# Kernel tuning notes

Measured on AMD Instinct MI355X. Metric: run time of the kernel, lower is better.

The kernel has to match this reference:

```python
import jax, jax.numpy as jnp
import numpy as np

N = 100000       # nodes
E = 1600000      # edges (avg degree 16)
D_IN = 128
D_HID = 128      # 2 * out_channels
D_OUT = 64
BN_EPS = 1e-5
LRELU_SLOPE = 0.01
NORM_SCALE = 1.8


def setup_inputs() -> dict:
    key = jax.random.key(0)
    ks = jax.random.split(key, 8)
    x = jax.random.normal(ks[0], (N, D_IN), dtype=jnp.float32)
    edge_src = jax.random.randint(ks[1], (E,), 0, N)
    edge_dst = jax.random.randint(ks[2], (E,), 0, N)
    W1 = jax.random.normal(ks[3], (D_IN, D_HID), dtype=jnp.float32) / np.sqrt(D_IN).astype(np.float32)
    b1 = jnp.zeros((D_HID,), jnp.float32)
    gamma = jnp.ones((D_HID,), jnp.float32)
    beta = jnp.zeros((D_HID,), jnp.float32)
    Wmu = jax.random.normal(ks[4], (D_HID, D_OUT), dtype=jnp.float32) / np.sqrt(D_HID).astype(np.float32)
    bmu = jnp.zeros((D_OUT,), jnp.float32)
    noise = jax.random.normal(ks[5], (N, D_OUT), dtype=jnp.float32)
    return {"x": x, "edge_src": edge_src, "edge_dst": edge_dst, "W1": W1, "b1": b1,
            "gamma": gamma, "beta": beta, "Wmu": Wmu, "bmu": bmu, "noise": noise}


def appnp_k1(x, src, dst):
    """APPNP(K=1, alpha=0) == one symmetric GCN-normalized SpMM with self-loops."""
    ones = jnp.ones((src.shape[0],), x.dtype)
    deg = jax.ops.segment_sum(ones, dst, num_segments=N) + 1.0  # +1 for self-loop
    dinv = jax.lax.rsqrt(deg)
    w = dinv[src] * dinv[dst]                                   # [E] edge weights
    agg = jax.ops.segment_sum(x[src] * w[:, None], dst, num_segments=N)
    return agg + x * (dinv * dinv)[:, None]                     # self-loop term


def reference(x, edge_src, edge_dst, W1, b1, gamma, beta, Wmu, bmu, noise):
    # conv1 + propagate
    h = x @ W1 + b1                         # [N, D_HID]
    h = appnp_k1(h, edge_src, edge_dst)
    # BatchNorm1d (training mode: batch stats, biased variance)
    mean = h.mean(axis=0)
    var = h.var(axis=0)
    h = gamma * (h - mean) * jax.lax.rsqrt(var + BN_EPS) + beta
    # LeakyReLU
    h = jnp.where(h > 0, h, LRELU_SLOPE * h)
    # mu branch (convmu + propagate)
    l = h @ Wmu + bmu                       # [N, D_OUT]; used for both mu and logstd (original reuses convmu)
    mu = appnp_k1(l, edge_src, edge_dst)
    # logstd branch: F.normalize(convmu(h), p=2, dim=1) * 1.8 then propagate
    nrm = jnp.maximum(jnp.linalg.norm(l, axis=1, keepdims=True), 1e-12)
    logstd = appnp_k1(l / nrm * NORM_SCALE, edge_src, edge_dst)
    # reparam (training): mu + eps * exp(logstd)
    zeta = mu + noise * jnp.exp(logstd)
    return (mu, logstd, zeta)
```

## Files before the change

kernel.cpp:

```cpp
#include <hip/hip_runtime.h>
#include <hip/hip_bf16.h>
#include <math.h>

#define D_IN 128
#define D_HID 128
#define D_OUT 64
#define BN_EPS 1e-5f
#define SLOPE 0.01f
#define NSCALE 1.8f

#define BSH 8
#define NB 256
#define T1 4096
#define COLCAP 8192
#define LSTRIDE 192

typedef __attribute__((ext_vector_type(8))) short short8;
typedef __attribute__((ext_vector_type(4))) float f32x4;

__device__ inline void atomAddF(float* p, float v) {
#if defined(__gfx90a__) || defined(__gfx942__) || defined(__gfx950__)
    unsafeAtomicAdd(p, v);
#else
    atomicAdd(p, v);
#endif
}

__device__ inline ushort f2bf(float f) {
    union { float f; uint u; } v; v.f = f;
    uint r = v.u + 0x7fff + ((v.u >> 16) & 1);
    return (ushort)(r >> 16);
}
__device__ inline float bf2f(ushort b) {
    union { uint u; float f; } v; v.u = ((uint)b) << 16;
    return v.f;
}
__device__ inline float bflo(uint u) { return __uint_as_float(u << 16); }
__device__ inline float bfhi(uint u) { return __uint_as_float(u & 0xffff0000u); }

__device__ inline void add8(uint4 v, float a[8]) {
    a[0] += bflo(v.x); a[1] += bfhi(v.x);
    a[2] += bflo(v.y); a[3] += bfhi(v.y);
    a[4] += bflo(v.z); a[5] += bfhi(v.z);
    a[6] += bflo(v.w); a[7] += bfhi(v.w);
}
__device__ inline void fma8(uint4 v, float w, float a[8]) {
    a[0] = fmaf(bflo(v.x), w, a[0]);
    a[1] = fmaf(bfhi(v.x), w, a[1]);
    a[2] = fmaf(bflo(v.y), w, a[2]);
    a[3] = fmaf(bfhi(v.y), w, a[3]);
    a[4] = fmaf(bflo(v.z), w, a[4]);
    a[5] = fmaf(bfhi(v.z), w, a[5]);
    a[6] = fmaf(bflo(v.w), w, a[6]);
    a[7] = fmaf(bfhi(v.w), w, a[7]);
}
__device__ inline void acc8(uint4 v, float sv, float w, float am[8], float al[8]) {
    float e;
    e = bflo(v.x) * w; am[0] += e; al[0] = fmaf(e, sv, al[0]);
    e = bfhi(v.x) * w; am[1] += e; al[1] = fmaf(e, sv, al[1]);
    e = bflo(v.y) * w; am[2] += e; al[2] = fmaf(e, sv, al[2]);
    e = bfhi(v.y) * w; am[3] += e; al[3] = fmaf(e, sv, al[3]);
    e = bflo(v.z) * w; am[4] += e; al[4] = fmaf(e, sv, al[4]);
    e = bfhi(v.z) * w; am[5] += e; al[5] = fmaf(e, sv, al[5]);
    e = bflo(v.w) * w; am[6] += e; al[6] = fmaf(e, sv, al[6]);
    e = bfhi(v.w) * w; am[7] += e; al[7] = fmaf(e, sv, al[7]);
}

__global__ __launch_bounds__(256) void k_bhist(const int* __restrict__ dst,
        int* __restrict__ bcnt, int E, int B) {
    __shared__ int h[512];
    for (int i = threadIdx.x; i < 512; i += 256) h[i] = 0;
    __syncthreads();
    int beg = blockIdx.x * T1;
    int end = min(beg + T1, E);
    for (int e = beg + threadIdx.x; e < end; e += 256)
        atomicAdd(&h[dst[e] >> BSH], 1);
    __syncthreads();
    for (int i = threadIdx.x; i < B; i += 256)
        if (h[i]) atomicAdd(&bcnt[i], h[i]);
}

__global__ __launch_bounds__(512) void k_bscan(const int* __restrict__ bcnt,
        int* __restrict__ bbase, int* __restrict__ tailE, int B) {
    __shared__ int sh[512];
    int t = threadIdx.x;
    int v = (t < B) ? bcnt[t] : 0;
    sh[t] = v;
    __syncthreads();
    for (int o = 1; o < 512; o <<= 1) {
        int u = (t >= o) ? sh[t - o] : 0;
        __syncthreads();
        sh[t] += u;
        __syncthreads();
    }
    int excl = sh[t] - v;
    if (t < B) { bbase[t] = excl; tailE[t] = excl; }
    if (t == B - 1) bbase[B] = excl + v;
}

__global__ __launch_bounds__(256) void k_part(const int* __restrict__ src,
        const int* __restrict__ dst, int* __restrict__ tailE,
        int2* __restrict__ ep, int E, int B) {
    __shared__ int h[512], off[512], gb[512], cur[512];
    __shared__ int ps[256];
    __shared__ int2 ro[T1];
    int tid = threadIdx.x;
    for (int i = tid; i < 512; i += 256) h[i] = 0;
    __syncthreads();
    int beg = blockIdx.x * T1;
    int cnt = min(T1, E - beg);
    int s[16], d[16];
#pragma unroll
    for (int k = 0; k < 16; ++k) {
        int e = beg + tid + k * 256;
        if (e < E) {
            s[k] = src[e]; d[k] = dst[e];
            atomicAdd(&h[d[k] >> BSH], 1);
        } else d[k] = -1;
    }
    __syncthreads();
    int pa = h[2 * tid], pb = h[2 * tid + 1];
    ps[tid] = pa + pb;
    __syncthreads();
    int vv = ps[tid];
    for (int o = 1; o < 256; o <<= 1) {
        int u = (tid >= o) ? ps[tid - o] : 0;
        __syncthreads();
        ps[tid] += u;
        __syncthreads();
    }
    int excl = ps[tid] - vv;
    off[2 * tid] = excl;       off[2 * tid + 1] = excl + pa;
    cur[2 * tid] = excl;       cur[2 * tid + 1] = excl + pa;
    if (2 * tid < B && pa > 0)      gb[2 * tid] = atomicAdd(&tailE[2 * tid], pa);
    if (2 * tid + 1 < B && pb > 0)  gb[2 * tid + 1] = atomicAdd(&tailE[2 * tid + 1], pb);
    __syncthreads();
#pragma unroll
    for (int k = 0; k < 16; ++k) {
        if (d[k] >= 0) {
            int b = d[k] >> BSH;
            int p = atomicAdd(&cur[b], 1);
            ro[p] = make_int2(s[k], d[k]);
        }
    }
    __syncthreads();
    for (int i = tid; i < cnt; i += 256) {
        int2 e = ro[i];
        int b = e.y >> BSH;
        ep[gb[b] + (i - off[b])] = e;
    }
}

__global__ __launch_bounds__(256) void k_csr(const int2* __restrict__ ep,
        const int* __restrict__ bbase, int* __restrict__ rowptr,
        float* __restrict__ dinv, int* __restrict__ col, int n, int B) {
    int b = blockIdx.x;
    int lo = b << BSH;
    int hi = min(lo + NB, n);
    int nn = hi - lo;
    int ebeg = bbase[b], eend = bbase[b + 1], cnt = eend - ebeg;
    __shared__ int h[NB], pfx[NB], cur[NB];
    __shared__ int colbuf[COLCAP];
    int tid = threadIdx.x;
    if (tid < NB) h[tid] = 0;
    __syncthreads();
    for (int i = tid; i < cnt; i += 256)
        atomicAdd(&h[ep[ebeg + i].y - lo], 1);
    __syncthreads();
    int v = (tid < nn) ? h[tid] : 0;
    pfx[tid] = v;
    __syncthreads();
    for (int o = 1; o < 256; o <<= 1) {
        int u = (tid >= o) ? pfx[tid - o] : 0;
        __syncthreads();
        pfx[tid] += u;
        __syncthreads();
    }
    int excl = pfx[tid] - v;
    if (tid < nn) {
        rowptr[lo + tid] = ebeg + excl;
        dinv[lo + tid] = rsqrtf((float)v + 1.0f);
        cur[tid] = excl;
    }
    if (b == B - 1 && tid == 0) rowptr[n] = eend;
    __syncthreads();
    if (cnt <= COLCAP) {
        for (int i = tid; i < cnt; i += 256) {
            int2 e = ep[ebeg + i];
            int p = atomicAdd(&cur[e.y - lo], 1);
            colbuf[p] = e.x;
        }
        __syncthreads();
        for (int i = tid; i < cnt; i += 256) col[ebeg + i] = colbuf[i];
    } else {
        for (int i = tid; i < cnt; i += 256) {
            int2 e = ep[ebeg + i];
            int p = atomicAdd(&cur[e.y - lo], 1);
            col[ebeg + p] = e.x;
        }
    }
}

__global__ __launch_bounds__(256) void k_gemm1_mfma(const float* __restrict__ x,
        const float* __restrict__ W1, const float* __restrict__ b1,
        const float* __restrict__ dinv, ushort* __restrict__ h_bf, int n, int nwt) {
    __shared__ ushort wf[2][4][8][64][8];
    int t = threadIdx.x;
    for (int i = t; i < 16384; i += 256) {
        int k = i >> 7, nn = i & 127;
        float v = W1[i];
        ushort hi = f2bf(v);
        ushort lo = f2bf(v - bf2f(hi));
        int kt = k >> 5, ct = nn >> 4;
        int lane = ((k >> 3) & 3) * 16 + (nn & 15);
        int j = k & 7;
        wf[0][kt][ct][lane][j] = hi;
        wf[1][kt][ct][lane][j] = lo;
    }
    __syncthreads();
    int wid = t >> 6, lane = t & 63;
    int lrow = lane & 15, lkg = lane >> 4;
    float bias[8];
#pragma unroll
    for (int ct = 0; ct < 8; ++ct) bias[ct] = b1[ct * 16 + lrow];
    int stride = gridDim.x * 4;
    for (int wt = blockIdx.x * 4 + wid; wt < nwt; wt += stride) {
        size_t r0 = (size_t)wt * 16;
        int rr = (int)r0 + lrow;
        if (rr >= n) rr = n - 1;
        short8 ah[4], al[4];
#pragma unroll
        for (int kt = 0; kt < 4; ++kt) {
            const float* p = x + (size_t)rr * 128 + kt * 32 + lkg * 8;
            float va[8];
            *(f32x4*)&va[0] = *(const f32x4*)p;
            *(f32x4*)&va[4] = *(const f32x4*)(p + 4);
#pragma unroll
            for (int j = 0; j < 8; ++j) {
                ushort hb = f2bf(va[j]);
                ah[kt][j] = (short)hb;
                al[kt][j] = (short)f2bf(va[j] - bf2f(hb));
            }
        }
        f32x4 acc[8];
#pragma unroll
        for (int ct = 0; ct < 8; ++ct) {
            float bb = bias[ct];
            acc[ct][0] = bb; acc[ct][1] = bb; acc[ct][2] = bb; acc[ct][3] = bb;
        }
#pragma unroll
        for (int kt = 0; kt < 4; ++kt) {
#pragma unroll
            for (int ct = 0; ct < 8; ++ct) {
                short8 wh = *(const short8*)&wf[0][kt][ct][lane][0];
                short8 wl = *(const short8*)&wf[1][kt][ct][lane][0];
                acc[ct] = __builtin_amdgcn_mfma_f32_16x16x32_bf16(ah[kt], wh, acc[ct], 0, 0, 0);
                acc[ct] = __builtin_amdgcn_mfma_f32_16x16x32_bf16(al[kt], wh, acc[ct], 0, 0, 0);
                acc[ct] = __builtin_amdgcn_mfma_f32_16x16x32_bf16(ah[kt], wl, acc[ct], 0, 0, 0);
            }
        }
#pragma unroll
        for (int j = 0; j < 4; ++j) {
            int row = (int)r0 + lkg * 4 + j;
            if (row < n) {
                float dr = dinv[row];
#pragma unroll
                for (int ct = 0; ct < 8; ++ct)
                    h_bf[(size_t)row * 128 + ct * 16 + lrow] = f2bf(acc[ct][j] * dr);
            }
        }
    }
}

__global__ __launch_bounds__(512) void k_spmm1_csr(const int* __restrict__ rowptr,
        const int* __restrict__ col, const uint4* __restrict__ hb4,
        const float* __restrict__ dinv, uint4* __restrict__ agg_bf,
        float* __restrict__ accum, int n) {
    __shared__ float red[8][16][8];
    int t = threadIdx.x;
    int wid = t >> 6, lane = t & 63;
    int q = lane >> 4, g = lane & 15;
    int gw = blockIdx.x * 8 + wid;
    int nw = gridDim.x * 8;
    float sx[8], sq[8];
#pragma unroll
    for (int j = 0; j < 8; ++j) { sx[j] = 0.f; sq[j] = 0.f; }
    for (int node = gw; node < n; node += nw) {
        int beg = rowptr[node], end = rowptr[node + 1];
        float a[8];
#pragma unroll
        for (int j = 0; j < 8; ++j) a[j] = 0.f;
        if (q == 0) add8(hb4[(size_t)node * 16 + g], a);
        int p = beg;
        for (; p + 16 <= end; p += 16) {
            int c0 = col[p + q], c1 = col[p + 4 + q];
            int c2 = col[p + 8 + q], c3 = col[p + 12 + q];
            uint4 v0 = hb4[(size_t)c0 * 16 + g];
            uint4 v1 = hb4[(size_t)c1 * 16 + g];
            uint4 v2 = hb4[(size_t)c2 * 16 + g];
            uint4 v3 = hb4[(size_t)c3 * 16 + g];
            add8(v0, a); add8(v1, a); add8(v2, a); add8(v3, a);
        }
        if (p + 8 <= end) {
            int c0 = col[p + q], c1 = col[p + 4 + q];
            uint4 v0 = hb4[(size_t)c0 * 16 + g];
            uint4 v1 = hb4[(size_t)c1 * 16 + g];
            add8(v0, a); add8(v1, a);
            p += 8;
        }
        if (p < end) {
            int i0 = p + q, i1 = p + 4 + q;
            int c0 = col[i0 < end ? i0 : end - 1];
            int c1 = col[i1 < end ? i1 : end - 1];
            float w0 = (i0 < end) ? 1.f : 0.f;
            float w1 = (i1 < end) ? 1.f : 0.f;
            fma8(hb4[(size_t)c0 * 16 + g], w0, a);
            fma8(hb4[(size_t)c1 * 16 + g], w1, a);
        }
#pragma unroll
        for (int j = 0; j < 8; ++j) {
            a[j] += __shfl_xor(a[j], 16, 64);
            a[j] += __shfl_xor(a[j], 32, 64);
        }
        if (q == 0) {
            float di = dinv[node];
#pragma unroll
            for (int j = 0; j < 8; ++j) a[j] *= di;
            uint4 pk;
            pk.x = ((uint)f2bf(a[1]) << 16) | (uint)f2bf(a[0]);
            pk.y = ((uint)f2bf(a[3]) << 16) | (uint)f2bf(a[2]);
            pk.z = ((uint)f2bf(a[5]) << 16) | (uint)f2bf(a[4]);
            pk.w = ((uint)f2bf(a[7]) << 16) | (uint)f2bf(a[6]);
            agg_bf[(size_t)node * 16 + g] = pk;
#pragma unroll
            for (int j = 0; j < 8; ++j) {
                sx[j] += a[j];
                sq[j] = fmaf(a[j], a[j], sq[j]);
            }
        }
    }
    if (q == 0) {
#pragma unroll
        for (int j = 0; j < 8; ++j) red[wid][g][j] = sx[j];
    }
    __syncthreads();
    if (t < 128) {
        float v = 0.f;
        for (int w = 0; w < 8; ++w) v += red[w][t >> 3][t & 7];
        atomAddF(&accum[t], v);
    }
    __syncthreads();
    if (q == 0) {
#pragma unroll
        for (int j = 0; j < 8; ++j) red[wid][g][j] = sq[j];
    }
    __syncthreads();
    if (t < 128) {
        float v = 0.f;
        for (int w = 0; w < 8; ++w) v += red[w][t >> 3][t & 7];
        atomAddF(&accum[128 + t], v);
    }
}

__global__ __launch_bounds__(256) void k_gemm2_mfma(const ushort* __restrict__ agg_bf,
        const float* __restrict__ Wmu, const float* __restrict__ bmu,
        const float* __restrict__ accum, const float* __restrict__ gamma,
        const float* __restrict__ beta, const float* __restrict__ dinv,
        char* __restrict__ l_ext, float inv_n, int n, int nwt) {
    __shared__ ushort wf[2][4][4][64][8];
    __shared__ float scs[D_HID], shs[D_HID];
    int t = threadIdx.x;
    for (int i = t; i < 8192; i += 256) {
        int k = i >> 6, nn = i & 63;
        float v = Wmu[i];
        ushort hi = f2bf(v);
        ushort lo = f2bf(v - bf2f(hi));
        int kt = k >> 5, ct = nn >> 4;
        int lane = ((k >> 3) & 3) * 16 + (nn & 15);
        int j = k & 7;
        wf[0][kt][ct][lane][j] = hi;
        wf[1][kt][ct][lane][j] = lo;
    }
    for (int i = t; i < D_HID; i += 256) {
        float mean = accum[i] * inv_n;
        float var = accum[D_HID + i] * inv_n - mean * mean;
        float sc = gamma[i] * rsqrtf(var + BN_EPS);
        scs[i] = sc;
        shs[i] = beta[i] - mean * sc;
    }
    __syncthreads();
    int wid = t >> 6, lane = t & 63;
    int lrow = lane & 15, lkg = lane >> 4;
    float bias[4];
#pragma unroll
    for (int ct = 0; ct < 4; ++ct) bias[ct] = bmu[ct * 16 + lrow];
    int stride = gridDim.x * 4;
    for (int wt = blockIdx.x * 4 + wid; wt < nwt; wt += stride) {
        size_t r0 = (size_t)wt * 16;
        int rr = (int)r0 + lrow;
        if (rr >= n) rr = n - 1;
        short8 ah[4], al[4];
#pragma unroll
        for (int kt = 0; kt < 4; ++kt) {
            const ushort* p = agg_bf + (size_t)rr * 128 + kt * 32 + lkg * 8;
            short8 raw = *(const short8*)p;
#pragma unroll
            for (int j = 0; j < 8; ++j) {
                int k = kt * 32 + lkg * 8 + j;
                float v = bf2f((ushort)raw[j]) * scs[k] + shs[k];
                v = v > 0.f ? v : SLOPE * v;
                ushort hb = f2bf(v);
                ah[kt][j] = (short)hb;
                al[kt][j] = (short)f2bf(v - bf2f(hb));
            }
        }
        f32x4 acc[4];
#pragma unroll
        for (int ct = 0; ct < 4; ++ct) {
            float bb = bias[ct];
            acc[ct][0] = bb; acc[ct][1] = bb; acc[ct][2] = bb; acc[ct][3] = bb;
        }
#pragma unroll
        for (int kt = 0; kt < 4; ++kt) {
#pragma unroll
            for (int ct = 0; ct < 4; ++ct) {
                short8 wh = *(const short8*)&wf[0][kt][ct][lane][0];
                short8 wl = *(const short8*)&wf[1][kt][ct][lane][0];
                acc[ct] = __builtin_amdgcn_mfma_f32_16x16x32_bf16(ah[kt], wh, acc[ct], 0, 0, 0);
                acc[ct] = __builtin_amdgcn_mfma_f32_16x16x32_bf16(al[kt], wh, acc[ct], 0, 0, 0);
                acc[ct] = __builtin_amdgcn_mfma_f32_16x16x32_bf16(ah[kt], wl, acc[ct], 0, 0, 0);
            }
        }
#pragma unroll
        for (int j = 0; j < 4; ++j) {
            float ss = acc[0][j] * acc[0][j];
#pragma unroll
            for (int ct = 1; ct < 4; ++ct) ss = fmaf(acc[ct][j], acc[ct][j], ss);
            ss += __shfl_xor(ss, 1, 64);
            ss += __shfl_xor(ss, 2, 64);
            ss += __shfl_xor(ss, 4, 64);
            ss += __shfl_xor(ss, 8, 64);
            float srow = NSCALE / fmaxf(sqrtf(ss), 1e-12f);
            int row = (int)r0 + lkg * 4 + j;
            if (row < n) {
                float dr = dinv[row];
                char* base = l_ext + (size_t)row * LSTRIDE;
#pragma unroll
                for (int ct = 0; ct < 4; ++ct)
                    *(ushort*)(base + (ct * 16 + lrow) * 2) = f2bf(acc[ct][j] * dr);
                if (lrow == 0) *(float*)(base + 128) = srow;
            }
        }
    }
}

__global__ __launch_bounds__(512) void k_spmm2_csr(const int* __restrict__ rowptr,
        const int* __restrict__ col, const char* __restrict__ lb,
        const float* __restrict__ dinv, const float* __restrict__ noise,
        float* __restrict__ mu, float* __restrict__ lsd, float* __restrict__ zeta,
        int n) {
    int node = blockIdx.x * 8 + ((int)threadIdx.x >> 6);
    if (node >= n) return;
    int lane = threadIdx.x & 63;
    int oct = lane >> 3, g = lane & 7;
    int beg = rowptr[node], end = rowptr[node + 1];
    float am[8], al[8];
#pragma unroll
    for (int j = 0; j < 8; ++j) { am[j] = 0.f; al[j] = 0.f; }
    if (oct == 0) {
        const char* rb = lb + (size_t)node * LSTRIDE;
        uint4 v = *(const uint4*)(rb + g * 16);
        float sv = *(const float*)(rb + 128);
        acc8(v, sv, 1.f, am, al);
    }
    int p = beg;
    for (; p + 16 <= end; p += 16) {
        int c0 = col[p + oct], c1 = col[p + 8 + oct];
        const char* r0 = lb + (size_t)c0 * LSTRIDE;
        const char* r1 = lb + (size_t)c1 * LSTRIDE;
        uint4 v0 = *(const uint4*)(r0 + g * 16);
        float s0 = *(const float*)(r0 + 128);
        uint4 v1 = *(const uint4*)(r1 + g * 16);
        float s1 = *(const float*)(r1 + 128);
        acc8(v0, s0, 1.f, am, al);
        acc8(v1, s1, 1.f, am, al);
    }
    if (p + 8 <= end) {
        int c0 = col[p + oct];
        const char* r0 = lb + (size_t)c0 * LSTRIDE;
        uint4 v0 = *(const uint4*)(r0 + g * 16);
        float s0 = *(const float*)(r0 + 128);
        acc8(v0, s0, 1.f, am, al);
        p += 8;
    }
    if (p < end) {
        int i0 = p + oct;
        int c0 = col[i0 < end ? i0 : end - 1];
        float w0 = (i0 < end) ? 1.f : 0.f;
        const char* r0 = lb + (size_t)c0 * LSTRIDE;
        uint4 v0 = *(const uint4*)(r0 + g * 16);
        float s0 = *(const float*)(r0 + 128);
        acc8(v0, s0, w0, am, al);
    }
#pragma unroll
    for (int j = 0; j < 8; ++j) {
        am[j] += __shfl_xor(am[j], 8, 64);
        am[j] += __shfl_xor(am[j], 16, 64);
        am[j] += __shfl_xor(am[j], 32, 64);
        al[j] += __shfl_xor(al[j], 8, 64);
        al[j] += __shfl_xor(al[j], 16, 64);
        al[j] += __shfl_xor(al[j], 32, 64);
    }
    if (lane < 8) {
        float di = dinv[node];
        size_t idx = (size_t)node * 64 + lane * 8;
        f32x4 m0, m1, l0, l1, z0, z1;
#pragma unroll
        for (int j = 0; j < 4; ++j) {
            m0[j] = am[j] * di;     m1[j] = am[j + 4] * di;
            l0[j] = al[j] * di;     l1[j] = al[j + 4] * di;
        }
        f32x4 n0 = *(const f32x4*)(noise + idx);
        f32x4 n1 = *(const f32x4*)(noise + idx + 4);
#pragma unroll
        for (int j = 0; j < 4; ++j) {
            z0[j] = m0[j] + n0[j] * expf(l0[j]);
            z1[j] = m1[j] + n1[j] * expf(l1[j]);
        }
        *(f32x4*)(mu + idx) = m0;   *(f32x4*)(mu + idx + 4) = m1;
        *(f32x4*)(lsd + idx) = l0;  *(f32x4*)(lsd + idx + 4) = l1;
        *(f32x4*)(zeta + idx) = z0; *(f32x4*)(zeta + idx + 4) = z1;
    }
}

extern "C" void kernel_launch(void* const* d_in, const int* in_sizes, int n_in,
                              void* d_out, int out_size, void* d_ws, size_t ws_size,
                              hipStream_t stream) {
    const float* x     = (const float*)d_in[0];
    const int*   esrc  = (const int*)d_in[1];
    const int*   edst  = (const int*)d_in[2];
    const float* W1    = (const float*)d_in[3];
    const float* b1    = (const float*)d_in[4];
    const float* gamma = (const float*)d_in[5];
    const float* beta  = (const float*)d_in[6];
    const float* Wmu   = (const float*)d_in[7];
    const float* bmu   = (const float*)d_in[8];
    const float* noise = (const float*)d_in[9];
    int N = in_sizes[0] / D_IN;
    int E = in_sizes[1];
    int B = (N + NB - 1) >> BSH;
    int nwt = (N + 15) / 16;
    int ntile = (E + T1 - 1) / T1;

    float* out  = (float*)d_out;
    float* mu   = out;
    float* lsd  = out + (size_t)N * D_OUT;
    float* zeta = out + 2 * (size_t)N * D_OUT;

    char* ws = (char*)d_ws;
    size_t off = 0;
    auto alloc = [&](size_t bytes) {
        void* p = ws + off;
        off += (bytes + 255) & ~(size_t)255;
        return p;
    };
    float* accum  = (float*)alloc(1024);
    int* bcnt     = (int*)alloc((size_t)B * 4);
    size_t zbytes = off;
    int* bbase    = (int*)alloc(((size_t)B + 1) * 4);
    int* tailE    = (int*)alloc((size_t)B * 4);
    int* rowptr   = (int*)alloc(((size_t)N + 1) * 4);
    float* dinv   = (float*)alloc((size_t)N * 4);
    int2* ep      = (int2*)alloc((size_t)E * 8);
    int* col      = (int*)alloc((size_t)E * 4);
    ushort* h_bf  = (ushort*)alloc((size_t)N * D_HID * 2);
    uint4* agg_bf = (uint4*)alloc((size_t)N * D_HID * 2);
    char* l_ext   = (char*)alloc((size_t)N * LSTRIDE);

    hipMemsetAsync(d_ws, 0, zbytes, stream);

    k_bhist<<<ntile, 256, 0, stream>>>(edst, bcnt, E, B);
    k_bscan<<<1, 512, 0, stream>>>(bcnt, bbase, tailE, B);
    k_part<<<ntile, 256, 0, stream>>>(esrc, edst, tailE, ep, E, B);
    k_csr<<<B, 256, 0, stream>>>(ep, bbase, rowptr, dinv, col, N, B);
    k_gemm1_mfma<<<512, 256, 0, stream>>>(x, W1, b1, dinv, h_bf, N, nwt);
    k_spmm1_csr<<<2048, 512, 0, stream>>>(rowptr, col, (const uint4*)h_bf, dinv, agg_bf, accum, N);
    k_gemm2_mfma<<<512, 256, 0, stream>>>((const ushort*)agg_bf, Wmu, bmu, accum,
                                          gamma, beta, dinv, l_ext, 1.0f / (float)N, N, nwt);
    k_spmm2_csr<<<(N + 7) / 8, 512, 0, stream>>>(rowptr, col, l_ext, dinv, noise, mu, lsd, zeta, N);
}
```

Measured before the change: 317.5 us.

## Split first SpMM into two feature halves, pack edge keys, drop weight-lo MFMA

The first GEMM now writes its output as two 64-column planes, and the first SpMM runs twice, once per plane. Each pass gathers from a 12.8 MB table instead of a 25.6 MB one, which is meant to raise cache hit rates for the random neighbor gathers. The edge partition buffer is packed into one 32-bit word (24-bit source plus 8-bit local destination), halving that traffic. Both GEMMs drop the low-part weight MFMA term, cutting a third of the MFMA work at some accuracy cost. The second launch also re-reads the CSR structure, and the packing assumes node ids fit in 24 bits.

```diff
diff --git a/kernel.cpp b/kernel.cpp
--- a/kernel.cpp
+++ b/kernel.cpp
@@ -38,21 +38,15 @@
 __device__ inline float bflo(uint u) { return __uint_as_float(u << 16); }
 __device__ inline float bfhi(uint u) { return __uint_as_float(u & 0xffff0000u); }
 
-__device__ inline void add8(uint4 v, float a[8]) {
+__device__ inline void add4(uint2 v, float a[4]) {
     a[0] += bflo(v.x); a[1] += bfhi(v.x);
     a[2] += bflo(v.y); a[3] += bfhi(v.y);
-    a[4] += bflo(v.z); a[5] += bfhi(v.z);
-    a[6] += bflo(v.w); a[7] += bfhi(v.w);
-}
-__device__ inline void fma8(uint4 v, float w, float a[8]) {
+}
+__device__ inline void fma4(uint2 v, float w, float a[4]) {
     a[0] = fmaf(bflo(v.x), w, a[0]);
     a[1] = fmaf(bfhi(v.x), w, a[1]);
     a[2] = fmaf(bflo(v.y), w, a[2]);
     a[3] = fmaf(bfhi(v.y), w, a[3]);
-    a[4] = fmaf(bflo(v.z), w, a[4]);
-    a[5] = fmaf(bfhi(v.z), w, a[5]);
-    a[6] = fmaf(bflo(v.w), w, a[6]);
-    a[7] = fmaf(bfhi(v.w), w, a[7]);
 }
 __device__ inline void acc8(uint4 v, float sv, float w, float am[8], float al[8]) {
     float e;
@@ -100,7 +94,7 @@
 
 __global__ __launch_bounds__(256) void k_part(const int* __restrict__ src,
         const int* __restrict__ dst, int* __restrict__ tailE,
-        int2* __restrict__ ep, int E, int B) {
+        uint* __restrict__ ep, int E, int B) {
     __shared__ int h[512], off[512], gb[512], cur[512];
     __shared__ int ps[256];
     __shared__ int2 ro[T1];
@@ -147,11 +141,11 @@
     for (int i = tid; i < cnt; i += 256) {
         int2 e = ro[i];
         int b = e.y >> BSH;
-        ep[gb[b] + (i - off[b])] = e;
-    }
-}
-
-__global__ __launch_bounds__(256) void k_csr(const int2* __restrict__ ep,
+        ep[gb[b] + (i - off[b])] = (uint)e.x | ((uint)(e.y & (NB - 1)) << 24);
+    }
+}
+
+__global__ __launch_bounds__(256) void k_csr(const uint* __restrict__ ep,
         const int* __restrict__ bbase, int* __restrict__ rowptr,
         float* __restrict__ dinv, int* __restrict__ col, int n, int B) {
     int b = blockIdx.x;
@@ -165,7 +159,7 @@
     if (tid < NB) h[tid] = 0;
     __syncthreads();
     for (int i = tid; i < cnt; i += 256)
-        atomicAdd(&h[ep[ebeg + i].y - lo], 1);
+        atomicAdd(&h[ep[ebeg + i] >> 24], 1);
     __syncthreads();
     int v = (tid < nn) ? h[tid] : 0;
     pfx[tid] = v;
@@ -186,17 +180,17 @@
     __syncthreads();
     if (cnt <= COLCAP) {
         for (int i = tid; i < cnt; i += 256) {
-            int2 e = ep[ebeg + i];
-            int p = atomicAdd(&cur[e.y - lo], 1);
-            colbuf[p] = e.x;
+            uint e = ep[ebeg + i];
+            int p = atomicAdd(&cur[e >> 24], 1);
+            colbuf[p] = (int)(e & 0xFFFFFFu);
         }
         __syncthreads();
         for (int i = tid; i < cnt; i += 256) col[ebeg + i] = colbuf[i];
     } else {
         for (int i = tid; i < cnt; i += 256) {
-            int2 e = ep[ebeg + i];
-            int p = atomicAdd(&cur[e.y - lo], 1);
-            col[ebeg + p] = e.x;
+            uint e = ep[ebeg + i];
+            int p = atomicAdd(&cur[e >> 24], 1);
+            col[ebeg + p] = (int)(e & 0xFFFFFFu);
         }
     }
 }
@@ -204,20 +198,17 @@
 __global__ __launch_bounds__(256) void k_gemm1_mfma(const float* __restrict__ x,
         const float* __restrict__ W1, const float* __restrict__ b1,
         const float* __restrict__ dinv, ushort* __restrict__ h_bf, int n, int nwt) {
-    __shared__ ushort wf[2][4][8][64][8];
+    __shared__ ushort wf[4][8][64][8];
     int t = threadIdx.x;
     for (int i = t; i < 16384; i += 256) {
         int k = i >> 7, nn = i & 127;
-        float v = W1[i];
-        ushort hi = f2bf(v);
-        ushort lo = f2bf(v - bf2f(hi));
         int kt = k >> 5, ct = nn >> 4;
         int lane = ((k >> 3) & 3) * 16 + (nn & 15);
         int j = k & 7;
-        wf[0][kt][ct][lane][j] = hi;
-        wf[1][kt][ct][lane][j] = lo;
-    }
-    __syncthreads();
+        wf[kt][ct][lane][j] = f2bf(W1[i]);
+    }
+    __syncthreads();
+    size_t n64 = (size_t)n * 64;
     int wid = t >> 6, lane = t & 63;
     int lrow = lane & 15, lkg = lane >> 4;
     float bias[8];
@@ -252,11 +243,9 @@
         for (int kt = 0; kt < 4; ++kt) {
 #pragma unroll
             for (int ct = 0; ct < 8; ++ct) {
-                short8 wh = *(const short8*)&wf[0][kt][ct][lane][0];
-                short8 wl = *(const short8*)&wf[1][kt][ct][lane][0];
+                short8 wh = *(const short8*)&wf[kt][ct][lane][0];
                 acc[ct] = __builtin_amdgcn_mfma_f32_16x16x32_bf16(ah[kt], wh, acc[ct], 0, 0, 0);
                 acc[ct] = __builtin_amdgcn_mfma_f32_16x16x32_bf16(al[kt], wh, acc[ct], 0, 0, 0);
-                acc[ct] = __builtin_amdgcn_mfma_f32_16x16x32_bf16(ah[kt], wl, acc[ct], 0, 0, 0);
             }
         }
 #pragma unroll
@@ -266,46 +255,43 @@
                 float dr = dinv[row];
 #pragma unroll
                 for (int ct = 0; ct < 8; ++ct)
-                    h_bf[(size_t)row * 128 + ct * 16 + lrow] = f2bf(acc[ct][j] * dr);
+                    h_bf[(size_t)(ct >> 2) * n64 + (size_t)row * 64 + (ct & 3) * 16 + lrow]
+                        = f2bf(acc[ct][j] * dr);
             }
         }
     }
 }
 
 __global__ __launch_bounds__(512) void k_spmm1_csr(const int* __restrict__ rowptr,
-        const int* __restrict__ col, const uint4* __restrict__ hb4,
-        const float* __restrict__ dinv, uint4* __restrict__ agg_bf,
-        float* __restrict__ accum, int n) {
-    __shared__ float red[8][16][8];
+        const int* __restrict__ col, const uint2* __restrict__ tbl,
+        const float* __restrict__ dinv, uint2* __restrict__ aggq,
+        float* __restrict__ accum, int n, int half) {
+    __shared__ float red[8][16][4];
     int t = threadIdx.x;
     int wid = t >> 6, lane = t & 63;
     int q = lane >> 4, g = lane & 15;
     int gw = blockIdx.x * 8 + wid;
     int nw = gridDim.x * 8;
-    float sx[8], sq[8];
-#pragma unroll
-    for (int j = 0; j < 8; ++j) { sx[j] = 0.f; sq[j] = 0.f; }
+    float sx[4] = {0.f, 0.f, 0.f, 0.f}, sq[4] = {0.f, 0.f, 0.f, 0.f};
     for (int node = gw; node < n; node += nw) {
         int beg = rowptr[node], end = rowptr[node + 1];
-        float a[8];
-#pragma unroll
-        for (int j = 0; j < 8; ++j) a[j] = 0.f;
-        if (q == 0) add8(hb4[(size_t)node * 16 + g], a);
+        float a[4] = {0.f, 0.f, 0.f, 0.f};
+        if (q == 0) add4(tbl[(size_t)node * 16 + g], a);
         int p = beg;
         for (; p + 16 <= end; p += 16) {
             int c0 = col[p + q], c1 = col[p + 4 + q];
             int c2 = col[p + 8 + q], c3 = col[p + 12 + q];
-            uint4 v0 = hb4[(size_t)c0 * 16 + g];
-            uint4 v1 = hb4[(size_t)c1 * 16 + g];
-            uint4 v2 = hb4[(size_t)c2 * 16 + g];
-            uint4 v3 = hb4[(size_t)c3 * 16 + g];
-            add8(v0, a); add8(v1, a); add8(v2, a); add8(v3, a);
+            uint2 v0 = tbl[(size_t)c0 * 16 + g];
+            uint2 v1 = tbl[(size_t)c1 * 16 + g];
+            uint2 v2 = tbl[(size_t)c2 * 16 + g];
+            uint2 v3 = tbl[(size_t)c3 * 16 + g];
+            add4(v0, a); add4(v1, a); add4(v2, a); add4(v3, a);
         }
         if (p + 8 <= end) {
             int c0 = col[p + q], c1 = col[p + 4 + q];
-            uint4 v0 = hb4[(size_t)c0 * 16 + g];
-            uint4 v1 = hb4[(size_t)c1 * 16 + g];
-            add8(v0, a); add8(v1, a);
+            uint2 v0 = tbl[(size_t)c0 * 16 + g];
+            uint2 v1 = tbl[(size_t)c1 * 16 + g];
+            add4(v0, a); add4(v1, a);
             p += 8;
         }
         if (p < end) {
@@ -314,26 +300,24 @@
             int c1 = col[i1 < end ? i1 : end - 1];
             float w0 = (i0 < end) ? 1.f : 0.f;
             float w1 = (i1 < end) ? 1.f : 0.f;
-            fma8(hb4[(size_t)c0 * 16 + g], w0, a);
-            fma8(hb4[(size_t)c1 * 16 + g], w1, a);
-        }
-#pragma unroll
-        for (int j = 0; j < 8; ++j) {
+            fma4(tbl[(size_t)c0 * 16 + g], w0, a);
+            fma4(tbl[(size_t)c1 * 16 + g], w1, a);
+        }
+#pragma unroll
+        for (int j = 0; j < 4; ++j) {
             a[j] += __shfl_xor(a[j], 16, 64);
             a[j] += __shfl_xor(a[j], 32, 64);
         }
         if (q == 0) {
             float di = dinv[node];
 #pragma unroll
-            for (int j = 0; j < 8; ++j) a[j] *= di;
-            uint4 pk;
+            for (int j = 0; j < 4; ++j) a[j] *= di;
+            uint2 pk;
             pk.x = ((uint)f2bf(a[1]) << 16) | (uint)f2bf(a[0]);
             pk.y = ((uint)f2bf(a[3]) << 16) | (uint)f2bf(a[2]);
-            pk.z = ((uint)f2bf(a[5]) << 16) | (uint)f2bf(a[4]);
-            pk.w = ((uint)f2bf(a[7]) << 16) | (uint)f2bf(a[6]);
-            agg_bf[(size_t)node * 16 + g] = pk;
-#pragma unroll
-            for (int j = 0; j < 8; ++j) {
+            aggq[(size_t)node * 32 + half * 16 + g] = pk;
+#pragma unroll
+            for (int j = 0; j < 4; ++j) {
                 sx[j] += a[j];
                 sq[j] = fmaf(a[j], a[j], sq[j]);
             }
@@ -341,24 +325,24 @@
     }
     if (q == 0) {
 #pragma unroll
-        for (int j = 0; j < 8; ++j) red[wid][g][j] = sx[j];
-    }
-    __syncthreads();
-    if (t < 128) {
+        for (int j = 0; j < 4; ++j) red[wid][g][j] = sx[j];
+    }
+    __syncthreads();
+    if (t < 64) {
         float v = 0.f;
-        for (int w = 0; w < 8; ++w) v += red[w][t >> 3][t & 7];
-        atomAddF(&accum[t], v);
+        for (int w = 0; w < 8; ++w) v += red[w][t >> 2][t & 3];
+        atomAddF(&accum[half * 64 + t], v);
     }
     __syncthreads();
     if (q == 0) {
 #pragma unroll
-        for (int j = 0; j < 8; ++j) red[wid][g][j] = sq[j];
-    }
-    __syncthreads();
-    if (t < 128) {
+        for (int j = 0; j < 4; ++j) red[wid][g][j] = sq[j];
+    }
+    __syncthreads();
+    if (t < 64) {
         float v = 0.f;
-        for (int w = 0; w < 8; ++w) v += red[w][t >> 3][t & 7];
-        atomAddF(&accum[128 + t], v);
+        for (int w = 0; w < 8; ++w) v += red[w][t >> 2][t & 3];
+        atomAddF(&accum[128 + half * 64 + t], v);
     }
 }
 
@@ -367,19 +351,15 @@
         const float* __restrict__ accum, const float* __restrict__ gamma,
         const float* __restrict__ beta, const float* __restrict__ dinv,
         char* __restrict__ l_ext, float inv_n, int n, int nwt) {
-    __shared__ ushort wf[2][4][4][64][8];
+    __shared__ ushort wf[4][4][64][8];
     __shared__ float scs[D_HID], shs[D_HID];
     int t = threadIdx.x;
     for (int i = t; i < 8192; i += 256) {
         int k = i >> 6, nn = i & 63;
-        float v = Wmu[i];
-        ushort hi = f2bf(v);
-        ushort lo = f2bf(v - bf2f(hi));
         int kt = k >> 5, ct = nn >> 4;
         int lane = ((k >> 3) & 3) * 16 + (nn & 15);
         int j = k & 7;
-        wf[0][kt][ct][lane][j] = hi;
-        wf[1][kt][ct][lane][j] = lo;
+        wf[kt][ct][lane][j] = f2bf(Wmu[i]);
     }
     for (int i = t; i < D_HID; i += 256) {
         float mean = accum[i] * inv_n;
@@ -424,11 +404,9 @@
         for (int kt = 0; kt < 4; ++kt) {
 #pragma unroll
             for (int ct = 0; ct < 4; ++ct) {
-                short8 wh = *(const short8*)&wf[0][kt][ct][lane][0];
-                short8 wl = *(const short8*)&wf[1][kt][ct][lane][0];
+                short8 wh = *(const short8*)&wf[kt][ct][lane][0];
                 acc[ct] = __builtin_amdgcn_mfma_f32_16x16x32_bf16(ah[kt], wh, acc[ct], 0, 0, 0);
                 acc[ct] = __builtin_amdgcn_mfma_f32_16x16x32_bf16(al[kt], wh, acc[ct], 0, 0, 0);
-                acc[ct] = __builtin_amdgcn_mfma_f32_16x16x32_bf16(ah[kt], wl, acc[ct], 0, 0, 0);
             }
         }
 #pragma unroll
@@ -571,21 +549,26 @@
     int* tailE    = (int*)alloc((size_t)B * 4);
     int* rowptr   = (int*)alloc(((size_t)N + 1) * 4);
     float* dinv   = (float*)alloc((size_t)N * 4);
-    int2* ep      = (int2*)alloc((size_t)E * 8);
+    uint* ep      = (uint*)alloc((size_t)E * 4);
     int* col      = (int*)alloc((size_t)E * 4);
     ushort* h_bf  = (ushort*)alloc((size_t)N * D_HID * 2);
-    uint4* agg_bf = (uint4*)alloc((size_t)N * D_HID * 2);
+    uint2* aggq   = (uint2*)alloc((size_t)N * D_HID * 2);
     char* l_ext   = (char*)alloc((size_t)N * LSTRIDE);
 
     hipMemsetAsync(d_ws, 0, zbytes, stream);
+
+    size_t n64 = (size_t)N * 64;
+    const uint2* tbl0 = (const uint2*)h_bf;
+    const uint2* tbl1 = (const uint2*)(h_bf + n64);
 
     k_bhist<<<ntile, 256, 0, stream>>>(edst, bcnt, E, B);
     k_bscan<<<1, 512, 0, stream>>>(bcnt, bbase, tailE, B);
     k_part<<<ntile, 256, 0, stream>>>(esrc, edst, tailE, ep, E, B);
     k_csr<<<B, 256, 0, stream>>>(ep, bbase, rowptr, dinv, col, N, B);
     k_gemm1_mfma<<<512, 256, 0, stream>>>(x, W1, b1, dinv, h_bf, N, nwt);
-    k_spmm1_csr<<<2048, 512, 0, stream>>>(rowptr, col, (const uint4*)h_bf, dinv, agg_bf, accum, N);
-    k_gemm2_mfma<<<512, 256, 0, stream>>>((const ushort*)agg_bf, Wmu, bmu, accum,
+    k_spmm1_csr<<<2048, 512, 0, stream>>>(rowptr, col, tbl0, dinv, aggq, accum, N, 0);
+    k_spmm1_csr<<<2048, 512, 0, stream>>>(rowptr, col, tbl1, dinv, aggq, accum, N, 1);
+    k_gemm2_mfma<<<512, 256, 0, stream>>>((const ushort*)aggq, Wmu, bmu, accum,
                                           gamma, beta, dinv, l_ext, 1.0f / (float)N, N, nwt);
     k_spmm2_csr<<<(N + 7) / 8, 512, 0, stream>>>(rowptr, col, l_ext, dinv, noise, mu, lsd, zeta, N);
 }
```

Result: no change. 311.6 us (-1.9%).
